# Optimization experiments

Hardware: AMD Instinct MI355X
Metric: run time of the kernel (lower is better)

Reference implementation:

```python
import jax, jax.numpy as jnp
import numpy as np

N, D = 8192, 128


def setup_inputs() -> dict:
    key = jax.random.key(0)
    k1, k2 = jax.random.split(key)
    emb = jax.random.normal(k1, (N, D), dtype=jnp.float32)
    graphWeight = jax.random.uniform(k2, (N, N), dtype=jnp.float32)
    return {"emb": emb, "graphWeight": graphWeight}


def _pairwise_l2(x):
    # cdist(x, x, p=2) via the ||a-b||^2 = ||a||^2 + ||b||^2 - 2 a.b identity.
    sq_norms = jnp.sum(x * x, axis=-1)  # [N]
    sq = sq_norms[:, None] + sq_norms[None, :] - 2.0 * (x @ x.T)  # [N, N]
    sq = jnp.maximum(sq, 0.0)
    # safe sqrt (grad-safe at exactly-zero distances, e.g. the diagonal)
    return jnp.where(sq > 0.0, jnp.sqrt(jnp.where(sq > 0.0, sq, 1.0)), 0.0)


def reference(emb, graphWeight):
    dist = _pairwise_l2(emb)                 # [N, N]
    dist = dist / jnp.max(dist)              # normalize by global max
    return jnp.mean((1.0 - dist) * graphWeight)  # scalar loss
```

## Files before the change

kernel.cpp:

```cpp
#include <hip/hip_runtime.h>
#include <hip/hip_bf16.h>

#define NN 8192
#define DD 128
#define JTPB 16

typedef __attribute__((ext_vector_type(8))) short short8;
typedef __attribute__((ext_vector_type(4))) float f32x4;

__device__ __forceinline__ unsigned short f2bf(float x) {
    unsigned u = __float_as_uint(x);
    u += 0x7FFFu + ((u >> 16) & 1u);
    return (unsigned short)(u >> 16);
}
__device__ __forceinline__ float bf2f(unsigned short b) {
    return __uint_as_float(((unsigned)b) << 16);
}

__device__ __forceinline__ void gld_lds16(const float* src, float* ldst) {
    __builtin_amdgcn_global_load_lds(
        (const __attribute__((address_space(1))) void*)src,
        (__attribute__((address_space(3))) void*)ldst, 16, 0, 0);
}

__global__ void prep_kernel(const float* __restrict__ emb,
                            unsigned short* __restrict__ ebf,
                            float* __restrict__ nrm) {
    int row  = blockIdx.x * 4 + (threadIdx.x >> 6);
    int lane = threadIdx.x & 63;
    const float2 v = *reinterpret_cast<const float2*>(emb + (size_t)row * DD + lane * 2);
    unsigned short b0 = f2bf(v.x), b1 = f2bf(v.y);
    ushort2 st; st.x = b0; st.y = b1;
    *reinterpret_cast<ushort2*>(ebf + (size_t)row * DD + lane * 2) = st;
    float f0 = bf2f(b0), f1 = bf2f(b1);
    float s = f0 * f0 + f1 * f1;
    #pragma unroll
    for (int m = 32; m; m >>= 1) s += __shfl_xor(s, m);
    if (lane == 0) nrm[row] = s;
}

__global__ __launch_bounds__(256)
void gram_kernel(const unsigned short* __restrict__ ebf,
                 const float* __restrict__ nrm,
                 const float* __restrict__ W,
                 float4* __restrict__ part) {
    __shared__ float wlds[2][64 * 128];
    __shared__ float sw_s[4], sdw_s[4], dm_s[4];

    const int wave = threadIdx.x >> 6;
    const int lane = threadIdx.x & 63;
    const int wRow = wave >> 1;
    const int wCol = wave & 1;
    const int i0  = blockIdx.y * 128;
    const int jc0 = blockIdx.x * (JTPB * 64);

    const int lr = lane & 15;
    const int hi = lane >> 4;
    const int lk = hi * 8;

    int pj[8], pc[8];
    #pragma unroll
    for (int r = 0; r < 8; ++r) {
        int q = r * 256 + (int)threadIdx.x;
        int jrow = q >> 5;
        pj[r] = jrow;
        pc[r] = ((q & 31) ^ (jrow & 7)) * 4;
    }

    short8 af[4][4];
    #pragma unroll
    for (int kc = 0; kc < 4; ++kc)
        #pragma unroll
        for (int m = 0; m < 4; ++m)
            af[kc][m] = *reinterpret_cast<const short8*>(
                ebf + (size_t)(i0 + wRow * 64 + m * 16 + lr) * DD + kc * 32 + lk);
    f32x4 ni4[4];
    #pragma unroll
    for (int m = 0; m < 4; ++m)
        ni4[m] = *reinterpret_cast<const f32x4*>(nrm + i0 + wRow * 64 + m * 16 + hi * 4);

    __builtin_amdgcn_sched_barrier(0);
    #pragma unroll
    for (int r = 0; r < 8; ++r)
        gld_lds16(W + (size_t)(jc0 + pj[r]) * NN + i0 + pc[r],
                  &wlds[0][r * 1024 + wave * 256]);
    __syncthreads();

    float sW = 0.f, sDW = 0.f, dmax = 0.f;

    for (int t = 0; t < JTPB; ++t) {
        const int j0t = jc0 + t * 64;
        const int jw  = j0t + wCol * 32;
        const int cb  = t & 1;

        short8 bf[4][2];
        #pragma unroll
        for (int kc = 0; kc < 4; ++kc)
            #pragma unroll
            for (int n = 0; n < 2; ++n)
                bf[kc][n] = *reinterpret_cast<const short8*>(
                    ebf + (size_t)(jw + n * 16 + lr) * DD + kc * 32 + lk);
        float nj[2];
        #pragma unroll
        for (int n = 0; n < 2; ++n) nj[n] = nrm[jw + n * 16 + lr];

        __builtin_amdgcn_sched_barrier(0);
        if (t + 1 < JTPB) {
            #pragma unroll
            for (int r = 0; r < 8; ++r)
                gld_lds16(W + (size_t)(j0t + 64 + pj[r]) * NN + i0 + pc[r],
                          &wlds[cb ^ 1][r * 1024 + wave * 256]);
        }
        __builtin_amdgcn_sched_barrier(0);

        f32x4 acc[4][2];
        #pragma unroll
        for (int m = 0; m < 4; ++m)
            #pragma unroll
            for (int n = 0; n < 2; ++n) acc[m][n] = (f32x4){0.f, 0.f, 0.f, 0.f};
        #pragma unroll
        for (int kc = 0; kc < 4; ++kc)
            #pragma unroll
            for (int m = 0; m < 4; ++m)
                #pragma unroll
                for (int n = 0; n < 2; ++n)
                    acc[m][n] = __builtin_amdgcn_mfma_f32_16x16x32_bf16(
                        af[kc][m], bf[kc][n], acc[m][n], 0, 0, 0);

        #pragma unroll
        for (int m = 0; m < 4; ++m) {
            #pragma unroll
            for (int n = 0; n < 2; ++n) {
                const int jp = wCol * 32 + n * 16 + lr;
                const int c0 = wRow * 16 + m * 4 + hi;
                const f32x4 w4 = *reinterpret_cast<const f32x4*>(
                    &wlds[cb][jp * 128 + ((c0 ^ (jp & 7)) * 4)]);
                #pragma unroll
                for (int r = 0; r < 4; ++r) {
                    float sq = ni4[m][r] + nj[n] - 2.0f * acc[m][n][r];
                    sq = fmaxf(sq, 0.0f);
                    float d = sqrtf(sq);
                    sW  += w4[r];
                    sDW += w4[r] * d;
                    dmax = fmaxf(dmax, d);
                }
            }
        }
        __syncthreads();
    }

    #pragma unroll
    for (int m = 32; m; m >>= 1) {
        sW  += __shfl_xor(sW, m);
        sDW += __shfl_xor(sDW, m);
        dmax = fmaxf(dmax, __shfl_xor(dmax, m));
    }
    if (lane == 0) { sw_s[wave] = sW; sdw_s[wave] = sDW; dm_s[wave] = dmax; }
    __syncthreads();
    if (threadIdx.x == 0) {
        float SW = 0.f, SDW = 0.f, DM = 0.f;
        #pragma unroll
        for (int k = 0; k < 4; ++k) {
            SW += sw_s[k]; SDW += sdw_s[k]; DM = fmaxf(DM, dm_s[k]);
        }
        float4 p; p.x = SW; p.y = SDW; p.z = DM; p.w = 0.f;
        part[blockIdx.y * gridDim.x + blockIdx.x] = p;
    }
}

__global__ __launch_bounds__(512)
void reduce_kernel(const float4* __restrict__ part, int nblk,
                   float* __restrict__ out) {
    const int tid = threadIdx.x;
    double sW = 0.0, sDW = 0.0;
    float dmax = 0.f;
    for (int idx = tid; idx < nblk; idx += 512) {
        float4 p = part[idx];
        sW += (double)p.x; sDW += (double)p.y; dmax = fmaxf(dmax, p.z);
    }
    #pragma unroll
    for (int m = 32; m; m >>= 1) {
        sW  += __shfl_xor(sW, m);
        sDW += __shfl_xor(sDW, m);
        dmax = fmaxf(dmax, __shfl_xor(dmax, m));
    }
    __shared__ double sw_s[8], sdw_s[8];
    __shared__ float dm_s[8];
    const int w = tid >> 6, l = tid & 63;
    if (l == 0) { sw_s[w] = sW; sdw_s[w] = sDW; dm_s[w] = dmax; }
    __syncthreads();
    if (tid == 0) {
        double SW = 0.0, SDW = 0.0; float DM = 0.f;
        #pragma unroll
        for (int k = 0; k < 8; ++k) {
            SW += sw_s[k]; SDW += sdw_s[k]; DM = fmaxf(DM, dm_s[k]);
        }
        out[0] = (float)((SW - SDW / (double)DM) / ((double)NN * (double)NN));
    }
}

extern "C" void kernel_launch(void* const* d_in, const int* in_sizes, int n_in,
                              void* d_out, int out_size, void* d_ws, size_t ws_size,
                              hipStream_t stream) {
    const float* emb = (const float*)d_in[0];
    const float* W   = (const float*)d_in[1];
    float* out = (float*)d_out;

    char* ws = (char*)d_ws;
    float4* part        = (float4*)ws;
    unsigned short* ebf = (unsigned short*)(ws + 16384);
    float* nrm          = (float*)(ws + 16384 + (size_t)NN * DD * 2);

    prep_kernel<<<NN / 4, 256, 0, stream>>>(emb, ebf, nrm);
    dim3 grid(NN / (64 * JTPB), NN / 128);
    gram_kernel<<<grid, 256, 0, stream>>>(ebf, nrm, W, part);
    reduce_kernel<<<1, 512, 0, stream>>>(part, grid.x * grid.y, out);
}
```

Measured before the change: 83.55 us.

## Replace LDS-direct W loads with nontemporal register staging and fuse final reduction

Loading of the weight matrix tiles changes from global_load_lds direct-to-LDS transfers to nontemporal global loads into registers, which are written to swizzled LDS after the MFMA/epilogue work of the current tile. The separate reduce kernel is removed: the last-finishing block, found with an atomic counter reset in prep_kernel, performs the final reduction, saving one launch. Launch bounds now request 2 blocks per CU. Register-staged prefetch costs extra VGPRs and may reduce overlap. The last-block pattern relies on threadfence/atomic ordering.

```diff
diff --git a/kernel.cpp b/kernel.cpp
--- a/kernel.cpp
+++ b/kernel.cpp
@@ -4,6 +4,7 @@
 #define NN 8192
 #define DD 128
 #define JTPB 16
+#define NBLK 512
 
 typedef __attribute__((ext_vector_type(8))) short short8;
 typedef __attribute__((ext_vector_type(4))) float f32x4;
@@ -17,15 +18,12 @@
     return __uint_as_float(((unsigned)b) << 16);
 }
 
-__device__ __forceinline__ void gld_lds16(const float* src, float* ldst) {
-    __builtin_amdgcn_global_load_lds(
-        (const __attribute__((address_space(1))) void*)src,
-        (__attribute__((address_space(3))) void*)ldst, 16, 0, 0);
-}
-
 __global__ void prep_kernel(const float* __restrict__ emb,
                             unsigned short* __restrict__ ebf,
-                            float* __restrict__ nrm) {
+                            float* __restrict__ nrm,
+                            unsigned int* __restrict__ done) {
+    if (blockIdx.x == 0 && threadIdx.x == 0)
+        __hip_atomic_store(done, 0u, __ATOMIC_RELAXED, __HIP_MEMORY_SCOPE_AGENT);
     int row  = blockIdx.x * 4 + (threadIdx.x >> 6);
     int lane = threadIdx.x & 63;
     const float2 v = *reinterpret_cast<const float2*>(emb + (size_t)row * DD + lane * 2);
@@ -39,13 +37,18 @@
     if (lane == 0) nrm[row] = s;
 }
 
-__global__ __launch_bounds__(256)
+__global__ __launch_bounds__(256, 2)
 void gram_kernel(const unsigned short* __restrict__ ebf,
                  const float* __restrict__ nrm,
                  const float* __restrict__ W,
-                 float4* __restrict__ part) {
+                 float4* __restrict__ part,
+                 unsigned int* __restrict__ done,
+                 float* __restrict__ out) {
     __shared__ float wlds[2][64 * 128];
     __shared__ float sw_s[4], sdw_s[4], dm_s[4];
+    __shared__ double swd[4], sdwd[4];
+    __shared__ float dmf[4];
+    __shared__ int last_s;
 
     const int wave = threadIdx.x >> 6;
     const int lane = threadIdx.x & 63;
@@ -58,14 +61,10 @@
     const int hi = lane >> 4;
     const int lk = hi * 8;
 
-    int pj[8], pc[8];
-    #pragma unroll
-    for (int r = 0; r < 8; ++r) {
-        int q = r * 256 + (int)threadIdx.x;
-        int jrow = q >> 5;
-        pj[r] = jrow;
-        pc[r] = ((q & 31) ^ (jrow & 7)) * 4;
-    }
+    const int trow = threadIdx.x >> 5;
+    const int tc   = threadIdx.x & 31;
+    const int swz4 = ((tc ^ trow) * 4);
+    const float* wbase = W + (size_t)i0 + tc * 4;
 
     short8 af[4][4];
     #pragma unroll
@@ -79,11 +78,16 @@
     for (int m = 0; m < 4; ++m)
         ni4[m] = *reinterpret_cast<const f32x4*>(nrm + i0 + wRow * 64 + m * 16 + hi * 4);
 
-    __builtin_amdgcn_sched_barrier(0);
-    #pragma unroll
-    for (int r = 0; r < 8; ++r)
-        gld_lds16(W + (size_t)(jc0 + pj[r]) * NN + i0 + pc[r],
-                  &wlds[0][r * 1024 + wave * 256]);
+    {
+        f32x4 w0[8];
+        #pragma unroll
+        for (int r = 0; r < 8; ++r)
+            w0[r] = __builtin_nontemporal_load(reinterpret_cast<const f32x4*>(
+                wbase + (size_t)(jc0 + r * 8 + trow) * NN));
+        #pragma unroll
+        for (int r = 0; r < 8; ++r)
+            *reinterpret_cast<f32x4*>(&wlds[0][(r * 8 + trow) * 128 + swz4]) = w0[r];
+    }
     __syncthreads();
 
     float sW = 0.f, sDW = 0.f, dmax = 0.f;
@@ -105,11 +109,13 @@
         for (int n = 0; n < 2; ++n) nj[n] = nrm[jw + n * 16 + lr];
 
         __builtin_amdgcn_sched_barrier(0);
-        if (t + 1 < JTPB) {
+        f32x4 wreg[8];
+        const bool more = (t + 1 < JTPB);
+        if (more) {
             #pragma unroll
             for (int r = 0; r < 8; ++r)
-                gld_lds16(W + (size_t)(j0t + 64 + pj[r]) * NN + i0 + pc[r],
-                          &wlds[cb ^ 1][r * 1024 + wave * 256]);
+                wreg[r] = __builtin_nontemporal_load(reinterpret_cast<const f32x4*>(
+                    wbase + (size_t)(j0t + 64 + r * 8 + trow) * NN));
         }
         __builtin_amdgcn_sched_barrier(0);
 
@@ -146,6 +152,14 @@
                 }
             }
         }
+
+        __builtin_amdgcn_sched_barrier(0);
+        if (more) {
+            float* dst = &wlds[cb ^ 1][0];
+            #pragma unroll
+            for (int r = 0; r < 8; ++r)
+                *reinterpret_cast<f32x4*>(&dst[(r * 8 + trow) * 128 + swz4]) = wreg[r];
+        }
         __syncthreads();
     }
 
@@ -157,6 +171,8 @@
     }
     if (lane == 0) { sw_s[wave] = sW; sdw_s[wave] = sDW; dm_s[wave] = dmax; }
     __syncthreads();
+
+    const int bid = blockIdx.y * gridDim.x + blockIdx.x;
     if (threadIdx.x == 0) {
         float SW = 0.f, SDW = 0.f, DM = 0.f;
         #pragma unroll
@@ -164,38 +180,40 @@
             SW += sw_s[k]; SDW += sdw_s[k]; DM = fmaxf(DM, dm_s[k]);
         }
         float4 p; p.x = SW; p.y = SDW; p.z = DM; p.w = 0.f;
-        part[blockIdx.y * gridDim.x + blockIdx.x] = p;
-    }
-}
-
-__global__ __launch_bounds__(512)
-void reduce_kernel(const float4* __restrict__ part, int nblk,
-                   float* __restrict__ out) {
-    const int tid = threadIdx.x;
-    double sW = 0.0, sDW = 0.0;
-    float dmax = 0.f;
-    for (int idx = tid; idx < nblk; idx += 512) {
-        float4 p = part[idx];
-        sW += (double)p.x; sDW += (double)p.y; dmax = fmaxf(dmax, p.z);
-    }
-    #pragma unroll
-    for (int m = 32; m; m >>= 1) {
-        sW  += __shfl_xor(sW, m);
-        sDW += __shfl_xor(sDW, m);
-        dmax = fmaxf(dmax, __shfl_xor(dmax, m));
-    }
-    __shared__ double sw_s[8], sdw_s[8];
-    __shared__ float dm_s[8];
-    const int w = tid >> 6, l = tid & 63;
-    if (l == 0) { sw_s[w] = sW; sdw_s[w] = sDW; dm_s[w] = dmax; }
+        part[bid] = p;
+        __threadfence();
+        unsigned prev = atomicAdd(done, 1u);
+        last_s = (prev == NBLK - 1) ? 1 : 0;
+    }
     __syncthreads();
-    if (tid == 0) {
-        double SW = 0.0, SDW = 0.0; float DM = 0.f;
-        #pragma unroll
-        for (int k = 0; k < 8; ++k) {
-            SW += sw_s[k]; SDW += sdw_s[k]; DM = fmaxf(DM, dm_s[k]);
-        }
-        out[0] = (float)((SW - SDW / (double)DM) / ((double)NN * (double)NN));
+
+    if (last_s) {
+        __threadfence();
+        double SW = 0.0, SDW = 0.0;
+        float DM = 0.f;
+        for (int idx = threadIdx.x; idx < NBLK; idx += 256) {
+            const float* p = reinterpret_cast<const float*>(part + idx);
+            float x = __hip_atomic_load(p + 0, __ATOMIC_RELAXED, __HIP_MEMORY_SCOPE_AGENT);
+            float y = __hip_atomic_load(p + 1, __ATOMIC_RELAXED, __HIP_MEMORY_SCOPE_AGENT);
+            float z = __hip_atomic_load(p + 2, __ATOMIC_RELAXED, __HIP_MEMORY_SCOPE_AGENT);
+            SW += (double)x; SDW += (double)y; DM = fmaxf(DM, z);
+        }
+        #pragma unroll
+        for (int m = 32; m; m >>= 1) {
+            SW  += __shfl_xor(SW, m);
+            SDW += __shfl_xor(SDW, m);
+            DM = fmaxf(DM, __shfl_xor(DM, m));
+        }
+        if (lane == 0) { swd[wave] = SW; sdwd[wave] = SDW; dmf[wave] = DM; }
+        __syncthreads();
+        if (threadIdx.x == 0) {
+            double TSW = 0.0, TSDW = 0.0; float TDM = 0.f;
+            #pragma unroll
+            for (int k = 0; k < 4; ++k) {
+                TSW += swd[k]; TSDW += sdwd[k]; TDM = fmaxf(TDM, dmf[k]);
+            }
+            out[0] = (float)((TSW - TSDW / (double)TDM) / ((double)NN * (double)NN));
+        }
     }
 }
 
@@ -208,11 +226,11 @@
 
     char* ws = (char*)d_ws;
     float4* part        = (float4*)ws;
+    unsigned int* done  = (unsigned int*)(ws + 8192);
     unsigned short* ebf = (unsigned short*)(ws + 16384);
     float* nrm          = (float*)(ws + 16384 + (size_t)NN * DD * 2);
 
-    prep_kernel<<<NN / 4, 256, 0, stream>>>(emb, ebf, nrm);
+    prep_kernel<<<NN / 4, 256, 0, stream>>>(emb, ebf, nrm, done);
     dim3 grid(NN / (64 * JTPB), NN / 128);
-    gram_kernel<<<grid, 256, 0, stream>>>(ebf, nrm, W, part);
-    reduce_kernel<<<1, 512, 0, stream>>>(part, grid.x * grid.y, out);
-}
+    gram_kernel<<<grid, 256, 0, stream>>>(ebf, nrm, W, part, done, out);
+}
```

Result: slower. 92.88 us (+11.2%).
